# Kernel optimization log

Measured on AMD Instinct MI355X. Metric: run time of the kernel, lower is better.

## Reference

```python
import jax, jax.numpy as jnp
import numpy as np

TABLE_SIZE = 524288   # power of 2: uint32 hash arithmetic matches torch int64 after mod
RESOLUTION = 512
FEAT_DIM = 4
N_POINTS = 4194304
PRIME_Y = jnp.uint32(2654435761)


def setup_inputs() -> dict:
    key = jax.random.key(0)
    k1, k2, k3, k4 = jax.random.split(key, 4)
    positions = jax.random.uniform(k1, (N_POINTS, 3), dtype=jnp.float32)  # in [0,1)
    table_xy = jax.random.normal(k2, (TABLE_SIZE, FEAT_DIM), dtype=jnp.float32) * 0.01
    table_xz = jax.random.normal(k3, (TABLE_SIZE, FEAT_DIM), dtype=jnp.float32) * 0.01
    table_yz = jax.random.normal(k4, (TABLE_SIZE, FEAT_DIM), dtype=jnp.float32) * 0.01
    return {"positions": positions, "table_xy": table_xy, "table_xz": table_xz, "table_yz": table_yz}


def _binarize_ste(t):
    # sign with zeros mapped to +1; STE: gradient is identity
    s = jnp.sign(t)
    b = s + (s == 0).astype(t.dtype)
    return t + jax.lax.stop_gradient(b - t)


_OFFSETS = jnp.array([[0, 0], [0, 1], [1, 0], [1, 1]], dtype=jnp.uint32)  # [4,2]


def _bilinear(pos2d, table):
    # pos2d: [N,2]
    scaled = pos2d * RESOLUTION
    floor_f = jnp.floor(scaled)
    w = scaled - floor_f                              # [N,2]
    corners = floor_f.astype(jnp.uint32)[:, None, :] + _OFFSETS[None]  # [N,4,2]
    # hash: x*1 ^ y*2654435761 mod table_size. uint32 wraparound equals torch int64
    # result because table_size is a power of two (only low bits matter).
    h = corners[..., 0] ^ (corners[..., 1] * PRIME_Y)  # [N,4] uint32
    idx = (h % jnp.uint32(TABLE_SIZE)).astype(jnp.int32)
    tab = _binarize_ste(table)                        # do_binarize=True (default)
    feats = tab[idx]                                  # [N,4,F] gather
    wx, wy = w[:, 0], w[:, 1]
    weights = jnp.stack([(1 - wx) * (1 - wy), (1 - wx) * wy,
                         wx * (1 - wy), wx * wy], axis=1)  # [N,4]
    return jnp.einsum('ncf,nc->nf', feats, weights)   # [N,F]


def reference(positions, table_xy, table_xz, table_yz):
    f_xy = _bilinear(positions[:, :2], table_xy)
    f_xz = _bilinear(positions[:, (0, 2)], table_xz)
    f_yz = _bilinear(positions[:, 1:3], table_yz)
    return f_xy + f_xz + f_yz
```

## Files before the change

### kernel.cpp

```cpp
#include <hip/hip_runtime.h>
#include <stdint.h>

#define TABLE_MASK 0x7FFFFu
#define PRIME 2654435761u
#define WORDS_PER_TABLE 65536
#define CELLS_PER_PLANE (512 * 512)

__global__ __launch_bounds__(256) void pack_kernel(
    const float* __restrict__ t0, const float* __restrict__ t1,
    const float* __restrict__ t2, uint32_t* __restrict__ out) {
  uint32_t tid = blockIdx.x * 256u + threadIdx.x;
  uint32_t tab = tid >> 16;
  uint32_t word = tid & 65535u;
  const float4* t =
      (const float4*)(tab == 0 ? t0 : (tab == 1 ? t1 : t2)) + word * 8u;
  uint32_t v = 0;
#pragma unroll
  for (int k = 0; k < 8; ++k) {
    float4 f = t[k];
    uint32_t n = (f.x >= 0.0f ? 1u : 0u) | (f.y >= 0.0f ? 2u : 0u) |
                 (f.z >= 0.0f ? 4u : 0u) | (f.w >= 0.0f ? 8u : 0u);
    v |= n << (4 * k);
  }
  out[tid] = v;
}

__global__ __launch_bounds__(256) void cellify_kernel(
    const uint32_t* __restrict__ pk, uint16_t* __restrict__ cells) {
  uint32_t tid = blockIdx.x * 256u + threadIdx.x;
  uint32_t plane = tid >> 18;
  uint32_t ia = (tid >> 9) & 511u;
  uint32_t ib = tid & 511u;
  const uint32_t* t = pk + plane * WORDS_PER_TABLE;
  uint32_t hb0 = ib * PRIME;
  uint32_t hb1 = hb0 + PRIME;
  uint32_t i00 = (ia ^ hb0) & TABLE_MASK;
  uint32_t i01 = (ia ^ hb1) & TABLE_MASK;
  uint32_t i10 = ((ia + 1u) ^ hb0) & TABLE_MASK;
  uint32_t i11 = ((ia + 1u) ^ hb1) & TABLE_MASK;
  uint32_t n00 = (t[i00 >> 3] >> ((i00 & 7u) * 4u)) & 15u;
  uint32_t n01 = (t[i01 >> 3] >> ((i01 & 7u) * 4u)) & 15u;
  uint32_t n10 = (t[i10 >> 3] >> ((i10 & 7u) * 4u)) & 15u;
  uint32_t n11 = (t[i11 >> 3] >> ((i11 & 7u) * 4u)) & 15u;
  cells[tid] = (uint16_t)(n00 | (n01 << 4) | (n10 << 8) | (n11 << 12));
}

__device__ __forceinline__ float bitmask_w(float w, uint32_t r, int bit) {
  return __uint_as_float(__float_as_uint(w) &
                         (uint32_t)__builtin_amdgcn_sbfe((int)r, bit, 1));
}

__global__ __launch_bounds__(256) void hash_main4(
    const float4* __restrict__ pos4, const uint16_t* __restrict__ cells,
    float4* __restrict__ out4, int nq) {
  int t = (int)(blockIdx.x * 256u + threadIdx.x);
  if (t >= nq) return;
  float4 A = pos4[3 * t + 0];
  float4 B = pos4[3 * t + 1];
  float4 C = pos4[3 * t + 2];
  float X[4] = {A.x, A.w, B.z, C.y};
  float Y[4] = {A.y, B.x, B.w, C.z};
  float Z[4] = {A.z, B.y, C.x, C.w};

  float WA[12], WB[12];
  uint32_t R[12];
#pragma unroll
  for (int k = 0; k < 4; ++k) {
    float pa[3] = {X[k], X[k], Y[k]};
    float pb[3] = {Y[k], Z[k], Z[k]};
#pragma unroll
    for (int p = 0; p < 3; ++p) {
      float sa = pa[p] * 512.0f, sb = pb[p] * 512.0f;
      float fa = floorf(sa), fb = floorf(sb);
      WA[3 * k + p] = sa - fa;
      WB[3 * k + p] = sb - fb;
      uint32_t ia = (uint32_t)fa, ib = (uint32_t)fb;
      R[3 * k + p] = cells[p * CELLS_PER_PLANE + ((ia << 9) | ib)];
    }
  }
#pragma unroll
  for (int k = 0; k < 4; ++k) {
    float q0 = 0.f, q1 = 0.f, q2 = 0.f, q3 = 0.f;
#pragma unroll
    for (int p = 0; p < 3; ++p) {
      uint32_t r = R[3 * k + p];
      float wa = WA[3 * k + p], wb = WB[3 * k + p];
      float omwa = 1.0f - wa, omwb = 1.0f - wb;
      float v00 = omwa * omwb, v01 = omwa * wb, v10 = wa * omwb, v11 = wa * wb;
      q0 += bitmask_w(v00, r, 0) + bitmask_w(v01, r, 4) +
            bitmask_w(v10, r, 8) + bitmask_w(v11, r, 12);
      q1 += bitmask_w(v00, r, 1) + bitmask_w(v01, r, 5) +
            bitmask_w(v10, r, 9) + bitmask_w(v11, r, 13);
      q2 += bitmask_w(v00, r, 2) + bitmask_w(v01, r, 6) +
            bitmask_w(v10, r, 10) + bitmask_w(v11, r, 14);
      q3 += bitmask_w(v00, r, 3) + bitmask_w(v01, r, 7) +
            bitmask_w(v10, r, 11) + bitmask_w(v11, r, 15);
    }
    float4 o;
    o.x = fmaf(2.0f, q0, -3.0f);
    o.y = fmaf(2.0f, q1, -3.0f);
    o.z = fmaf(2.0f, q2, -3.0f);
    o.w = fmaf(2.0f, q3, -3.0f);
    out4[4 * t + k] = o;
  }
}

__device__ __forceinline__ void plane_cell(
    const uint16_t* __restrict__ cells, float a, float b,
    float& p0, float& p1, float& p2, float& p3) {
  float sa = a * 512.0f, sb = b * 512.0f;
  float fa = floorf(sa), fb = floorf(sb);
  float wa = sa - fa, wb = sb - fb;
  uint32_t ia = (uint32_t)fa, ib = (uint32_t)fb;
  uint32_t r = cells[(ia << 9) | ib];
  float omwa = 1.0f - wa, omwb = 1.0f - wb;
  float v00 = omwa * omwb, v01 = omwa * wb, v10 = wa * omwb, v11 = wa * wb;
  p0 += bitmask_w(v00, r, 0) + bitmask_w(v01, r, 4) + bitmask_w(v10, r, 8) +
        bitmask_w(v11, r, 12);
  p1 += bitmask_w(v00, r, 1) + bitmask_w(v01, r, 5) + bitmask_w(v10, r, 9) +
        bitmask_w(v11, r, 13);
  p2 += bitmask_w(v00, r, 2) + bitmask_w(v01, r, 6) + bitmask_w(v10, r, 10) +
        bitmask_w(v11, r, 14);
  p3 += bitmask_w(v00, r, 3) + bitmask_w(v01, r, 7) + bitmask_w(v10, r, 11) +
        bitmask_w(v11, r, 15);
}

__global__ __launch_bounds__(256) void hash_tail(
    const float* __restrict__ pos, const uint16_t* __restrict__ cells,
    float4* __restrict__ out, int n, int start) {
  int i = start + (int)(blockIdx.x * 256u + threadIdx.x);
  if (i >= n) return;
  float x = pos[3 * i + 0];
  float y = pos[3 * i + 1];
  float z = pos[3 * i + 2];
  float p0 = 0.f, p1 = 0.f, p2 = 0.f, p3 = 0.f;
  plane_cell(cells, x, y, p0, p1, p2, p3);
  plane_cell(cells + CELLS_PER_PLANE, x, z, p0, p1, p2, p3);
  plane_cell(cells + 2 * CELLS_PER_PLANE, y, z, p0, p1, p2, p3);
  float4 o;
  o.x = fmaf(2.0f, p0, -3.0f);
  o.y = fmaf(2.0f, p1, -3.0f);
  o.z = fmaf(2.0f, p2, -3.0f);
  o.w = fmaf(2.0f, p3, -3.0f);
  out[i] = o;
}

__device__ __forceinline__ void plane_accum(
    const uint32_t* __restrict__ t, float a, float b,
    float& p0, float& p1, float& p2, float& p3) {
  float sa = a * 512.0f, sb = b * 512.0f;
  float fa = floorf(sa), fb = floorf(sb);
  float wa = sa - fa, wb = sb - fb;
  uint32_t ia = (uint32_t)fa, ib = (uint32_t)fb;
  uint32_t hb0 = ib * PRIME;
  uint32_t hb1 = hb0 + PRIME;
  uint32_t i00 = (ia ^ hb0) & TABLE_MASK;
  uint32_t i01 = (ia ^ hb1) & TABLE_MASK;
  uint32_t d = ia ^ (ia + 1u);
  uint32_t i10 = i00 ^ d;
  uint32_t i11 = i01 ^ d;
  uint32_t w00 = t[i00 >> 3];
  uint32_t w01 = t[i01 >> 3];
  uint32_t w10 = w00, w11 = w01;
  if (d >= 8u) {
    w10 = t[i10 >> 3];
    w11 = t[i11 >> 3];
  }
  uint32_t n00 = w00 >> ((i00 & 7u) * 4u);
  uint32_t n01 = w01 >> ((i01 & 7u) * 4u);
  uint32_t n10 = w10 >> ((i10 & 7u) * 4u);
  uint32_t n11 = w11 >> ((i11 & 7u) * 4u);
  float omwa = 1.0f - wa, omwb = 1.0f - wb;
  float v00 = omwa * omwb, v01 = omwa * wb, v10 = wa * omwb, v11 = wa * wb;
  p0 += bitmask_w(v00, n00, 0) + bitmask_w(v01, n01, 0) +
        bitmask_w(v10, n10, 0) + bitmask_w(v11, n11, 0);
  p1 += bitmask_w(v00, n00, 1) + bitmask_w(v01, n01, 1) +
        bitmask_w(v10, n10, 1) + bitmask_w(v11, n11, 1);
  p2 += bitmask_w(v00, n00, 2) + bitmask_w(v01, n01, 2) +
        bitmask_w(v10, n10, 2) + bitmask_w(v11, n11, 2);
  p3 += bitmask_w(v00, n00, 3) + bitmask_w(v01, n01, 3) +
        bitmask_w(v10, n10, 3) + bitmask_w(v11, n11, 3);
}

__global__ __launch_bounds__(256) void hash_packed(
    const float* __restrict__ pos, const uint32_t* __restrict__ pk,
    float4* __restrict__ out, int n) {
  int i = (int)(blockIdx.x * 256u + threadIdx.x);
  if (i >= n) return;
  float x = pos[3 * i + 0];
  float y = pos[3 * i + 1];
  float z = pos[3 * i + 2];
  float p0 = 0.f, p1 = 0.f, p2 = 0.f, p3 = 0.f;
  plane_accum(pk, x, y, p0, p1, p2, p3);
  plane_accum(pk + WORDS_PER_TABLE, x, z, p0, p1, p2, p3);
  plane_accum(pk + 2 * WORDS_PER_TABLE, y, z, p0, p1, p2, p3);
  float4 o;
  o.x = fmaf(2.0f, p0, -3.0f);
  o.y = fmaf(2.0f, p1, -3.0f);
  o.z = fmaf(2.0f, p2, -3.0f);
  o.w = fmaf(2.0f, p3, -3.0f);
  out[i] = o;
}

extern "C" void kernel_launch(void* const* d_in, const int* in_sizes, int n_in,
                              void* d_out, int out_size, void* d_ws,
                              size_t ws_size, hipStream_t stream) {
  const float* pos = (const float*)d_in[0];
  const float* txy = (const float*)d_in[1];
  const float* txz = (const float*)d_in[2];
  const float* tyz = (const float*)d_in[3];
  float4* out = (float4*)d_out;
  int n = in_sizes[0] / 3;
  const size_t pk_bytes = (size_t)3 * WORDS_PER_TABLE * 4;
  const size_t cell_bytes = (size_t)3 * CELLS_PER_PLANE * 2;
  if (ws_size >= pk_bytes + cell_bytes) {
    uint32_t* pk = (uint32_t*)d_ws;
    uint16_t* cells = (uint16_t*)((char*)d_ws + pk_bytes);
    pack_kernel<<<3 * WORDS_PER_TABLE / 256, 256, 0, stream>>>(txy, txz, tyz,
                                                               pk);
    cellify_kernel<<<3 * CELLS_PER_PLANE / 256, 256, 0, stream>>>(pk, cells);
    int nq = n / 4;
    if (nq > 0)
      hash_main4<<<(nq + 255) / 256, 256, 0, stream>>>(
          (const float4*)pos, cells, out, nq);
    int rem = n - nq * 4;
    if (rem > 0)
      hash_tail<<<(rem + 255) / 256, 256, 0, stream>>>(pos, cells, out, n,
                                                       nq * 4);
  } else {
    uint32_t* pk = (uint32_t*)d_ws;
    pack_kernel<<<3 * WORDS_PER_TABLE / 256, 256, 0, stream>>>(txy, txz, tyz,
                                                               pk);
    hash_packed<<<(n + 255) / 256, 256, 0, stream>>>(pos, pk, out, n);
  }
}
```

Baseline: 185.4 us.

## Stage XY-plane corner nibbles in LDS, keep cell lookups for XZ/YZ

Adds a per-corner nibble grid for the XY plane (513x513 corners, about 132KB) that each 1024-thread block copies into LDS. The XY lookup then reads four corner nibbles from LDS, while the XZ and YZ planes still use precomputed 16-bit cell records in global memory. The goal is to cut one of the three random global gathers per point. The cost is a large per-block LDS fill, which limits occupancy to one block per CU. The old packed-only fallback path is removed.

```diff
diff --git a/kernel.cpp b/kernel.cpp
--- a/kernel.cpp
+++ b/kernel.cpp
@@ -5,6 +5,8 @@
 #define PRIME 2654435761u
 #define WORDS_PER_TABLE 65536
 #define CELLS_PER_PLANE (512 * 512)
+#define CORNER_DWORDS 32961
+#define CORNER_BYTES (CORNER_DWORDS * 4)
 
 __global__ __launch_bounds__(256) void pack_kernel(
     const float* __restrict__ t0, const float* __restrict__ t1,
@@ -23,6 +25,134 @@
     v |= n << (4 * k);
   }
   out[tid] = v;
+}
+
+__global__ __launch_bounds__(256) void cellify2_kernel(
+    const uint32_t* __restrict__ pk, uint16_t* __restrict__ cells2) {
+  uint32_t tid = blockIdx.x * 256u + threadIdx.x;
+  uint32_t pp = tid >> 18;
+  uint32_t ia = (tid >> 9) & 511u;
+  uint32_t ib = tid & 511u;
+  const uint32_t* t = pk + (pp + 1) * WORDS_PER_TABLE;
+  uint32_t hb0 = ib * PRIME;
+  uint32_t hb1 = hb0 + PRIME;
+  uint32_t i00 = (ia ^ hb0) & TABLE_MASK;
+  uint32_t i01 = (ia ^ hb1) & TABLE_MASK;
+  uint32_t d = ia ^ (ia + 1u);
+  uint32_t i10 = i00 ^ d;
+  uint32_t i11 = i01 ^ d;
+  uint32_t w00 = t[i00 >> 3];
+  uint32_t w01 = t[i01 >> 3];
+  uint32_t w10 = w00, w11 = w01;
+  if (d >= 8u) {
+    w10 = t[i10 >> 3];
+    w11 = t[i11 >> 3];
+  }
+  uint32_t n00 = (w00 >> ((i00 & 7u) * 4u)) & 15u;
+  uint32_t n01 = (w01 >> ((i01 & 7u) * 4u)) & 15u;
+  uint32_t n10 = (w10 >> ((i10 & 7u) * 4u)) & 15u;
+  uint32_t n11 = (w11 >> ((i11 & 7u) * 4u)) & 15u;
+  cells2[tid] = (uint16_t)(n00 | (n01 << 4) | (n10 << 8) | (n11 << 12));
+}
+
+__global__ __launch_bounds__(256) void corner_kernel(
+    const uint32_t* __restrict__ pk, uint32_t* __restrict__ cornerg) {
+  uint32_t t = blockIdx.x * 256u + threadIdx.x;
+  if (t >= CORNER_DWORDS) return;
+  uint32_t d = 0;
+#pragma unroll
+  for (int k = 0; k < 8; ++k) {
+    uint32_t ci = 8u * t + (uint32_t)k;
+    uint32_t ix = ci / 514u;
+    uint32_t iy = ci - 514u * ix;
+    uint32_t nib = 0;
+    if (iy <= 512u) {
+      uint32_t idx = (ix ^ (iy * PRIME)) & TABLE_MASK;
+      nib = (pk[idx >> 3] >> ((idx & 7u) * 4u)) & 15u;
+    }
+    d |= nib << (4 * k);
+  }
+  cornerg[t] = d;
+}
+
+__device__ __forceinline__ float bitmask_w(float w, uint32_t r, int bit) {
+  return __uint_as_float(__float_as_uint(w) &
+                         (uint32_t)__builtin_amdgcn_sbfe((int)r, bit, 1));
+}
+
+__device__ __forceinline__ void acc_rec(uint32_t r, float wa, float wb,
+                                        float& q0, float& q1, float& q2,
+                                        float& q3) {
+  float omwa = 1.0f - wa, omwb = 1.0f - wb;
+  float v00 = omwa * omwb, v01 = omwa * wb, v10 = wa * omwb, v11 = wa * wb;
+  q0 += bitmask_w(v00, r, 0) + bitmask_w(v01, r, 4) + bitmask_w(v10, r, 8) +
+        bitmask_w(v11, r, 12);
+  q1 += bitmask_w(v00, r, 1) + bitmask_w(v01, r, 5) + bitmask_w(v10, r, 9) +
+        bitmask_w(v11, r, 13);
+  q2 += bitmask_w(v00, r, 2) + bitmask_w(v01, r, 6) + bitmask_w(v10, r, 10) +
+        bitmask_w(v11, r, 14);
+  q3 += bitmask_w(v00, r, 3) + bitmask_w(v01, r, 7) + bitmask_w(v10, r, 11) +
+        bitmask_w(v11, r, 15);
+}
+
+__global__ __launch_bounds__(1024, 1) void hash_lds(
+    const float4* __restrict__ pos4, const uint16_t* __restrict__ cells2,
+    const uint32_t* __restrict__ cornerg, float4* __restrict__ out4, int nq) {
+  extern __shared__ uint32_t lds4[];
+  for (int j = (int)threadIdx.x; j < CORNER_DWORDS; j += 1024)
+    lds4[j] = cornerg[j];
+  __syncthreads();
+  int t = (int)(blockIdx.x * 1024u + threadIdx.x);
+  if (t >= nq) return;
+  float4 A = pos4[3 * t + 0];
+  float4 B = pos4[3 * t + 1];
+  float4 C = pos4[3 * t + 2];
+  float X[4] = {A.x, A.w, B.z, C.y};
+  float Y[4] = {A.y, B.x, B.w, C.z};
+  float Z[4] = {A.z, B.y, C.x, C.w};
+
+  float WAxz[4], WByz[4], WAyz[4], WZ[4];
+  uint32_t Gxz[4], Gyz[4];
+#pragma unroll
+  for (int k = 0; k < 4; ++k) {
+    float sx = X[k] * 512.0f, sy = Y[k] * 512.0f, sz = Z[k] * 512.0f;
+    float fx = floorf(sx), fy = floorf(sy), fz = floorf(sz);
+    uint32_t ix = (uint32_t)fx, iy = (uint32_t)fy, iz = (uint32_t)fz;
+    WAxz[k] = sx - fx;
+    WAyz[k] = sy - fy;
+    WZ[k] = sz - fz;
+    WByz[k] = WZ[k];
+    Gxz[k] = cells2[(ix << 9) | iz];
+    Gyz[k] = cells2[CELLS_PER_PLANE + ((iy << 9) | iz)];
+  }
+  __builtin_amdgcn_sched_barrier(0);
+
+  const uint8_t* lb = (const uint8_t*)lds4;
+#pragma unroll
+  for (int k = 0; k < 4; ++k) {
+    float sa = X[k] * 512.0f, sb = Y[k] * 512.0f;
+    float fa = floorf(sa), fb = floorf(sb);
+    float wa = sa - fa, wb = sb - fb;
+    uint32_t ia = (uint32_t)fa, ib = (uint32_t)fb;
+    uint32_t r0 = ia * 257u, r1 = r0 + 257u;
+    uint32_t c0 = ib >> 1, c1 = (ib + 1u) >> 1;
+    uint32_t s0 = (ib & 1u) * 4u, s1 = ((ib + 1u) & 1u) * 4u;
+    uint32_t n00 = ((uint32_t)lb[r0 + c0] >> s0) & 15u;
+    uint32_t n01 = ((uint32_t)lb[r0 + c1] >> s1) & 15u;
+    uint32_t n10 = ((uint32_t)lb[r1 + c0] >> s0) & 15u;
+    uint32_t n11 = ((uint32_t)lb[r1 + c1] >> s1) & 15u;
+    uint32_t rxy = n00 | (n01 << 4) | (n10 << 8) | (n11 << 12);
+    float q0 = 0.f, q1 = 0.f, q2 = 0.f, q3 = 0.f;
+    acc_rec(rxy, wa, wb, q0, q1, q2, q3);
+    acc_rec(Gxz[k], WAxz[k], WZ[k], q0, q1, q2, q3);
+    acc_rec(Gyz[k], WAyz[k], WByz[k], q0, q1, q2, q3);
+    float4 o;
+    o.x = fmaf(2.0f, q0, -3.0f);
+    o.y = fmaf(2.0f, q1, -3.0f);
+    o.z = fmaf(2.0f, q2, -3.0f);
+    o.w = fmaf(2.0f, q3, -3.0f);
+    out4[4 * t + k] = o;
+  }
 }
 
 __global__ __launch_bounds__(256) void cellify_kernel(
@@ -45,11 +175,6 @@
   cells[tid] = (uint16_t)(n00 | (n01 << 4) | (n10 << 8) | (n11 << 12));
 }
 
-__device__ __forceinline__ float bitmask_w(float w, uint32_t r, int bit) {
-  return __uint_as_float(__float_as_uint(w) &
-                         (uint32_t)__builtin_amdgcn_sbfe((int)r, bit, 1));
-}
-
 __global__ __launch_bounds__(256) void hash_main4(
     const float4* __restrict__ pos4, const uint16_t* __restrict__ cells,
     float4* __restrict__ out4, int nq) {
@@ -61,7 +186,6 @@
   float X[4] = {A.x, A.w, B.z, C.y};
   float Y[4] = {A.y, B.x, B.w, C.z};
   float Z[4] = {A.z, B.y, C.x, C.w};
-
   float WA[12], WB[12];
   uint32_t R[12];
 #pragma unroll
@@ -82,20 +206,8 @@
   for (int k = 0; k < 4; ++k) {
     float q0 = 0.f, q1 = 0.f, q2 = 0.f, q3 = 0.f;
 #pragma unroll
-    for (int p = 0; p < 3; ++p) {
-      uint32_t r = R[3 * k + p];
-      float wa = WA[3 * k + p], wb = WB[3 * k + p];
-      float omwa = 1.0f - wa, omwb = 1.0f - wb;
-      float v00 = omwa * omwb, v01 = omwa * wb, v10 = wa * omwb, v11 = wa * wb;
-      q0 += bitmask_w(v00, r, 0) + bitmask_w(v01, r, 4) +
-            bitmask_w(v10, r, 8) + bitmask_w(v11, r, 12);
-      q1 += bitmask_w(v00, r, 1) + bitmask_w(v01, r, 5) +
-            bitmask_w(v10, r, 9) + bitmask_w(v11, r, 13);
-      q2 += bitmask_w(v00, r, 2) + bitmask_w(v01, r, 6) +
-            bitmask_w(v10, r, 10) + bitmask_w(v11, r, 14);
-      q3 += bitmask_w(v00, r, 3) + bitmask_w(v01, r, 7) +
-            bitmask_w(v10, r, 11) + bitmask_w(v11, r, 15);
-    }
+    for (int p = 0; p < 3; ++p)
+      acc_rec(R[3 * k + p], WA[3 * k + p], WB[3 * k + p], q0, q1, q2, q3);
     float4 o;
     o.x = fmaf(2.0f, q0, -3.0f);
     o.y = fmaf(2.0f, q1, -3.0f);
@@ -103,26 +215,6 @@
     o.w = fmaf(2.0f, q3, -3.0f);
     out4[4 * t + k] = o;
   }
-}
-
-__device__ __forceinline__ void plane_cell(
-    const uint16_t* __restrict__ cells, float a, float b,
-    float& p0, float& p1, float& p2, float& p3) {
-  float sa = a * 512.0f, sb = b * 512.0f;
-  float fa = floorf(sa), fb = floorf(sb);
-  float wa = sa - fa, wb = sb - fb;
-  uint32_t ia = (uint32_t)fa, ib = (uint32_t)fb;
-  uint32_t r = cells[(ia << 9) | ib];
-  float omwa = 1.0f - wa, omwb = 1.0f - wb;
-  float v00 = omwa * omwb, v01 = omwa * wb, v10 = wa * omwb, v11 = wa * wb;
-  p0 += bitmask_w(v00, r, 0) + bitmask_w(v01, r, 4) + bitmask_w(v10, r, 8) +
-        bitmask_w(v11, r, 12);
-  p1 += bitmask_w(v00, r, 1) + bitmask_w(v01, r, 5) + bitmask_w(v10, r, 9) +
-        bitmask_w(v11, r, 13);
-  p2 += bitmask_w(v00, r, 2) + bitmask_w(v01, r, 6) + bitmask_w(v10, r, 10) +
-        bitmask_w(v11, r, 14);
-  p3 += bitmask_w(v00, r, 3) + bitmask_w(v01, r, 7) + bitmask_w(v10, r, 11) +
-        bitmask_w(v11, r, 15);
 }
 
 __global__ __launch_bounds__(256) void hash_tail(
@@ -133,72 +225,32 @@
   float x = pos[3 * i + 0];
   float y = pos[3 * i + 1];
   float z = pos[3 * i + 2];
-  float p0 = 0.f, p1 = 0.f, p2 = 0.f, p3 = 0.f;
-  plane_cell(cells, x, y, p0, p1, p2, p3);
-  plane_cell(cells + CELLS_PER_PLANE, x, z, p0, p1, p2, p3);
-  plane_cell(cells + 2 * CELLS_PER_PLANE, y, z, p0, p1, p2, p3);
+  float q0 = 0.f, q1 = 0.f, q2 = 0.f, q3 = 0.f;
+  {
+    float sa = x * 512.0f, sb = y * 512.0f;
+    float fa = floorf(sa), fb = floorf(sb);
+    uint32_t ia = (uint32_t)fa, ib = (uint32_t)fb;
+    acc_rec(cells[(ia << 9) | ib], sa - fa, sb - fb, q0, q1, q2, q3);
+  }
+  {
+    float sa = x * 512.0f, sb = z * 512.0f;
+    float fa = floorf(sa), fb = floorf(sb);
+    uint32_t ia = (uint32_t)fa, ib = (uint32_t)fb;
+    acc_rec(cells[CELLS_PER_PLANE + ((ia << 9) | ib)], sa - fa, sb - fb, q0,
+            q1, q2, q3);
+  }
+  {
+    float sa = y * 512.0f, sb = z * 512.0f;
+    float fa = floorf(sa), fb = floorf(sb);
+    uint32_t ia = (uint32_t)fa, ib = (uint32_t)fb;
+    acc_rec(cells[2 * CELLS_PER_PLANE + ((ia << 9) | ib)], sa - fa, sb - fb,
+            q0, q1, q2, q3);
+  }
   float4 o;
-  o.x = fmaf(2.0f, p0, -3.0f);
-  o.y = fmaf(2.0f, p1, -3.0f);
-  o.z = fmaf(2.0f, p2, -3.0f);
-  o.w = fmaf(2.0f, p3, -3.0f);
-  out[i] = o;
-}
-
-__device__ __forceinline__ void plane_accum(
-    const uint32_t* __restrict__ t, float a, float b,
-    float& p0, float& p1, float& p2, float& p3) {
-  float sa = a * 512.0f, sb = b * 512.0f;
-  float fa = floorf(sa), fb = floorf(sb);
-  float wa = sa - fa, wb = sb - fb;
-  uint32_t ia = (uint32_t)fa, ib = (uint32_t)fb;
-  uint32_t hb0 = ib * PRIME;
-  uint32_t hb1 = hb0 + PRIME;
-  uint32_t i00 = (ia ^ hb0) & TABLE_MASK;
-  uint32_t i01 = (ia ^ hb1) & TABLE_MASK;
-  uint32_t d = ia ^ (ia + 1u);
-  uint32_t i10 = i00 ^ d;
-  uint32_t i11 = i01 ^ d;
-  uint32_t w00 = t[i00 >> 3];
-  uint32_t w01 = t[i01 >> 3];
-  uint32_t w10 = w00, w11 = w01;
-  if (d >= 8u) {
-    w10 = t[i10 >> 3];
-    w11 = t[i11 >> 3];
-  }
-  uint32_t n00 = w00 >> ((i00 & 7u) * 4u);
-  uint32_t n01 = w01 >> ((i01 & 7u) * 4u);
-  uint32_t n10 = w10 >> ((i10 & 7u) * 4u);
-  uint32_t n11 = w11 >> ((i11 & 7u) * 4u);
-  float omwa = 1.0f - wa, omwb = 1.0f - wb;
-  float v00 = omwa * omwb, v01 = omwa * wb, v10 = wa * omwb, v11 = wa * wb;
-  p0 += bitmask_w(v00, n00, 0) + bitmask_w(v01, n01, 0) +
-        bitmask_w(v10, n10, 0) + bitmask_w(v11, n11, 0);
-  p1 += bitmask_w(v00, n00, 1) + bitmask_w(v01, n01, 1) +
-        bitmask_w(v10, n10, 1) + bitmask_w(v11, n11, 1);
-  p2 += bitmask_w(v00, n00, 2) + bitmask_w(v01, n01, 2) +
-        bitmask_w(v10, n10, 2) + bitmask_w(v11, n11, 2);
-  p3 += bitmask_w(v00, n00, 3) + bitmask_w(v01, n01, 3) +
-        bitmask_w(v10, n10, 3) + bitmask_w(v11, n11, 3);
-}
-
-__global__ __launch_bounds__(256) void hash_packed(
-    const float* __restrict__ pos, const uint32_t* __restrict__ pk,
-    float4* __restrict__ out, int n) {
-  int i = (int)(blockIdx.x * 256u + threadIdx.x);
-  if (i >= n) return;
-  float x = pos[3 * i + 0];
-  float y = pos[3 * i + 1];
-  float z = pos[3 * i + 2];
-  float p0 = 0.f, p1 = 0.f, p2 = 0.f, p3 = 0.f;
-  plane_accum(pk, x, y, p0, p1, p2, p3);
-  plane_accum(pk + WORDS_PER_TABLE, x, z, p0, p1, p2, p3);
-  plane_accum(pk + 2 * WORDS_PER_TABLE, y, z, p0, p1, p2, p3);
-  float4 o;
-  o.x = fmaf(2.0f, p0, -3.0f);
-  o.y = fmaf(2.0f, p1, -3.0f);
-  o.z = fmaf(2.0f, p2, -3.0f);
-  o.w = fmaf(2.0f, p3, -3.0f);
+  o.x = fmaf(2.0f, q0, -3.0f);
+  o.y = fmaf(2.0f, q1, -3.0f);
+  o.z = fmaf(2.0f, q2, -3.0f);
+  o.w = fmaf(2.0f, q3, -3.0f);
   out[i] = o;
 }
 
@@ -212,8 +264,32 @@
   float4* out = (float4*)d_out;
   int n = in_sizes[0] / 3;
   const size_t pk_bytes = (size_t)3 * WORDS_PER_TABLE * 4;
-  const size_t cell_bytes = (size_t)3 * CELLS_PER_PLANE * 2;
-  if (ws_size >= pk_bytes + cell_bytes) {
+  const size_t cell2_bytes = (size_t)2 * CELLS_PER_PLANE * 2;
+  const size_t cell3_bytes = (size_t)3 * CELLS_PER_PLANE * 2;
+  const size_t lds_bytes = (size_t)CORNER_BYTES;
+
+  bool lds_ok = (n % 4096 == 0) &&
+                ws_size >= pk_bytes + cell2_bytes + CORNER_BYTES;
+  if (lds_ok) {
+    hipError_t e = hipFuncSetAttribute(
+        (const void*)hash_lds, hipFuncAttributeMaxDynamicSharedMemorySize,
+        (int)lds_bytes);
+    if (e != hipSuccess) lds_ok = false;
+  }
+
+  if (lds_ok) {
+    uint32_t* pk = (uint32_t*)d_ws;
+    uint16_t* cells2 = (uint16_t*)((char*)d_ws + pk_bytes);
+    uint32_t* cornerg = (uint32_t*)((char*)d_ws + pk_bytes + cell2_bytes);
+    pack_kernel<<<3 * WORDS_PER_TABLE / 256, 256, 0, stream>>>(txy, txz, tyz,
+                                                               pk);
+    cellify2_kernel<<<2 * CELLS_PER_PLANE / 256, 256, 0, stream>>>(pk, cells2);
+    corner_kernel<<<(CORNER_DWORDS + 255) / 256, 256, 0, stream>>>(pk,
+                                                                   cornerg);
+    int nq = n / 4;
+    hash_lds<<<(nq + 1023) / 1024, 1024, lds_bytes, stream>>>(
+        (const float4*)pos, cells2, cornerg, out, nq);
+  } else if (ws_size >= pk_bytes + cell3_bytes) {
     uint32_t* pk = (uint32_t*)d_ws;
     uint16_t* cells = (uint16_t*)((char*)d_ws + pk_bytes);
     pack_kernel<<<3 * WORDS_PER_TABLE / 256, 256, 0, stream>>>(txy, txz, tyz,
@@ -221,16 +297,11 @@
     cellify_kernel<<<3 * CELLS_PER_PLANE / 256, 256, 0, stream>>>(pk, cells);
     int nq = n / 4;
     if (nq > 0)
-      hash_main4<<<(nq + 255) / 256, 256, 0, stream>>>(
-          (const float4*)pos, cells, out, nq);
+      hash_main4<<<(nq + 255) / 256, 256, 0, stream>>>((const float4*)pos,
+                                                       cells, out, nq);
     int rem = n - nq * 4;
     if (rem > 0)
       hash_tail<<<(rem + 255) / 256, 256, 0, stream>>>(pos, cells, out, n,
                                                        nq * 4);
-  } else {
-    uint32_t* pk = (uint32_t*)d_ws;
-    pack_kernel<<<3 * WORDS_PER_TABLE / 256, 256, 0, stream>>>(txy, txz, tyz,
-                                                               pk);
-    hash_packed<<<(n + 255) / 256, 256, 0, stream>>>(pos, pk, out, n);
-  }
-}
+  }
+}
```

Result: no change. 183.4 us (-1.1%).
